# Optimization experiments

Measured on AMD Instinct MI355X. Metric: run time of the kernel, lower is better.

Reference implementation:

```python
import jax, jax.numpy as jnp
import numpy as np

N0, N1 = 20000, 20000     # users, items
F0 = 512                  # raw feature dim per type
HID = 64                  # hidden_dim == H * D
H, D = 8, 8               # num_heads, out_dim
P = 2                     # metapaths per side
E = 200000                # metapath instances per metapath
L = 3                     # metapath length (nodes)
B = 8192                  # link-prediction target batch
AV = 128                  # attn_vec_dim
CH = 128                  # ProductMLP hidden = max(128, HID//2)
ETYPES_USER = [[0, 1], [0, 1]]
ETYPES_ITEM = [[1, 0], [1, 0]]


def setup_inputs() -> dict:
    key = jax.random.key(0)
    ks = jax.random.split(key, 32)
    def nrm(k, shape, fan_in):
        return (jax.random.normal(k, shape, dtype=jnp.float32) * (1.414 / np.sqrt(fan_in))).astype(jnp.float32)
    inp = {}
    inp['feats0'] = jax.random.normal(ks[0], (N0, F0), dtype=jnp.float32)
    inp['feats1'] = jax.random.normal(ks[1], (N1, F0), dtype=jnp.float32)
    for t, off in ((0, 2), (1, 6)):
        inp[f'tower{t}_pw'] = nrm(ks[off], (F0, HID), F0)
        inp[f'tower{t}_pb'] = jnp.zeros((HID,), jnp.float32)
        inp[f'tower{t}_w2'] = nrm(ks[off + 1], (HID, HID), HID)
        inp[f'tower{t}_b2'] = jnp.zeros((HID,), jnp.float32)
        inp[f'tower{t}_g'] = jnp.ones((HID,), jnp.float32)
        inp[f'tower{t}_be'] = jnp.zeros((HID,), jnp.float32)
    inp['r_vec'] = jax.random.normal(ks[10], (2, HID // 2, 2), dtype=jnp.float32)
    inp['attn_user'] = nrm(ks[11], (P, H, D), D)
    inp['attn_item'] = nrm(ks[12], (P, H, D), D)
    inp['su_w1'] = nrm(ks[13], (HID, AV), HID)
    inp['su_b1'] = jnp.zeros((AV,), jnp.float32)
    inp['su_w2'] = nrm(ks[14], (AV,), AV)
    inp['si_w1'] = nrm(ks[15], (HID, AV), HID)
    inp['si_b1'] = jnp.zeros((AV,), jnp.float32)
    inp['si_w2'] = nrm(ks[16], (AV,), AV)
    inp['cw1'] = nrm(ks[17], (HID, CH), HID)
    inp['cb1'] = jnp.zeros((CH,), jnp.float32)
    inp['cw2'] = nrm(ks[18], (CH, 2), CH)
    inp['idx0'] = jnp.arange(N0, dtype=jnp.int32)
    inp['idx1'] = jnp.arange(N1, dtype=jnp.int32) + N0
    inp['emi_user'] = jax.random.randint(ks[20], (P, E, L), 0, N0 + N1, dtype=jnp.int32)
    inp['tgt_user'] = jax.random.randint(ks[21], (P, E), 0, B, dtype=jnp.int32)
    inp['emi_item'] = jax.random.randint(ks[22], (P, E, L), 0, N0 + N1, dtype=jnp.int32)
    inp['tgt_item'] = jax.random.randint(ks[23], (P, E), 0, B, dtype=jnp.int32)
    return inp


def _tower(x, pw, pb, w2, b2, g, be):
    # Linear -> GELU -> Linear -> residual -> LayerNorm (dropout off in eval)
    z = x @ pw + pb
    h = jax.nn.gelu(z, approximate=False)
    h = h @ w2 + b2
    y = h + z
    mu = y.mean(-1, keepdims=True)
    var = ((y - mu) ** 2).mean(-1, keepdims=True)
    return (y - mu) / jnp.sqrt(var + 1e-5) * g + be


def _rot_full(r_vec):
    # normalize to unit complex, then even etypes = r, odd etypes = conj(r)
    r = r_vec / jnp.linalg.norm(r_vec, axis=-1, keepdims=True)
    conj = r * jnp.array([1.0, -1.0], dtype=r.dtype)
    return jnp.stack([r, conj], axis=1).reshape(-1, r.shape[1], 2)  # [num_edge_type, HID//2, 2]


def _final_r(rfull, etypes):
    # cumulative complex rotation applied to each position along the metapath
    fr = [None] * L
    fr[L - 1] = jnp.stack([jnp.ones(HID // 2), jnp.zeros(HID // 2)], axis=1).astype(rfull.dtype)
    for i in range(L - 2, -1, -1):
        rv = rfull[etypes[i]]
        re = fr[i + 1][:, 0] * rv[:, 0] - fr[i + 1][:, 1] * rv[:, 1]
        im = fr[i + 1][:, 0] * rv[:, 1] + fr[i + 1][:, 1] * rv[:, 0]
        fr[i] = jnp.stack([re, im], axis=1)
    return jnp.stack(fr)  # [L, HID//2, 2]


def _metapath(feat, emi, tgt, attn, etypes, rfull):
    # gather node features along each metapath instance: [E, L, HID//2, 2]
    ed = feat[emi].reshape(emi.shape[0], L, HID // 2, 2)
    fr = _final_r(rfull, etypes)  # last position is identity rotation
    re = ed[..., 0] * fr[:, :, 0] - ed[..., 1] * fr[:, :, 1]
    im = ed[..., 0] * fr[:, :, 1] + ed[..., 1] * fr[:, :, 0]
    hidden = jnp.stack([re, im], -1).mean(axis=1).reshape(-1, HID)  # mean over metapath positions
    eft = hidden.reshape(-1, H, D)
    e = jax.nn.leaky_relu((eft * attn).sum(-1), 0.01)  # [E, H]
    # edge softmax over instances sharing a target node
    m = jax.ops.segment_max(e, tgt, num_segments=B)
    m = jnp.where(jnp.isfinite(m), m, 0.0)
    a = jnp.exp(e - m[tgt])
    s = jax.ops.segment_sum(a, tgt, num_segments=B)
    w = a / (s[tgt] + 1e-9)
    ret = jax.ops.segment_sum(w[..., None] * eft, tgt, num_segments=B)  # [B, H, D]
    return jax.nn.elu(ret.reshape(B, HID))


def _semantic(outs, w1, b1, w2):
    hs = jnp.stack(outs)  # [P, B, HID]
    s = (jnp.tanh(hs @ w1 + b1) @ w2).mean(axis=1)  # [P]
    beta = jax.nn.softmax(s)
    return (beta[:, None, None] * hs).sum(0)  # [B, HID]


def reference(feats0, feats1, tower0_pw, tower0_pb, tower0_w2, tower0_b2, tower0_g, tower0_be,
              tower1_pw, tower1_pb, tower1_w2, tower1_b2, tower1_g, tower1_be,
              r_vec, attn_user, attn_item, su_w1, su_b1, su_w2, si_w1, si_b1, si_w2,
              cw1, cb1, cw2, idx0, idx1, emi_user, tgt_user, emi_item, tgt_item):
    t0 = _tower(feats0, tower0_pw, tower0_pb, tower0_w2, tower0_b2, tower0_g, tower0_be)
    t1 = _tower(feats1, tower1_pw, tower1_pb, tower1_w2, tower1_b2, tower1_g, tower1_be)
    feat = jnp.zeros((N0 + N1, HID), jnp.float32).at[idx0].set(t0).at[idx1].set(t1)
    rfull = _rot_full(r_vec)
    user_outs = [_metapath(feat, emi_user[p], tgt_user[p], attn_user[p], ETYPES_USER[p], rfull) for p in range(P)]
    item_outs = [_metapath(feat, emi_item[p], tgt_item[p], attn_item[p], ETYPES_ITEM[p], rfull) for p in range(P)]
    h_user = _semantic(user_outs, su_w1, su_b1, su_w2)
    h_item = _semantic(item_outs, si_w1, si_b1, si_w2)
    x = h_user * h_item
    h = jax.nn.relu(x @ cw1 + cb1)
    logits = h @ cw2
    return jax.nn.softmax(logits, axis=-1)
```

## Files before the change

### kernel.cpp

```cpp
#include <hip/hip_runtime.h>
#include <hip/hip_bf16.h>
#include <math.h>

#define NN0 20000
#define NN1 20000
#define NTOT 40000
#define FF0 512
#define HIDD 64
#define EEE 200000
#define BBB 8192
#define AVV 128
#define CHH 128

typedef __bf16 bf16x8 __attribute__((ext_vector_type(8)));
typedef __bf16 bf16x4 __attribute__((ext_vector_type(4)));
typedef float f32x4 __attribute__((ext_vector_type(4)));
typedef float f32x2 __attribute__((ext_vector_type(2)));

__device__ __forceinline__ float fast_tanh(float x) {
    float e2 = __expf(2.f * x);
    return 1.f - 2.f / (e2 + 1.f);
}

__device__ __forceinline__ f32x2 bf2_to_f32x2(unsigned int c) {
    f32x2 r;
    r.x = __uint_as_float(c << 16);
    r.y = __uint_as_float(c & 0xffff0000u);
    return r;
}

__device__ __forceinline__ void coarse_prefix(const int* __restrict__ cnt32p, int combo, int tid,
                                              int& cv, int& excl) {
    cv = cnt32p[(combo * 32 + tid) * 32];
    int pre = cv;
#pragma unroll
    for (int d = 1; d < 32; d <<= 1) {
        int o = __shfl_up(pre, d);
        if (tid >= d) pre += o;
    }
    excl = pre - cv;
}

#define HCHUNK 1024
__global__ __launch_bounds__(256) void prep_hist(
    const float* __restrict__ pw0, const float* __restrict__ pw1,
    const float* __restrict__ w20, const float* __restrict__ w21,
    __bf16* __restrict__ wprep, __bf16* __restrict__ w2prep,
    const int* __restrict__ tgt_user, const int* __restrict__ tgt_item,
    int* __restrict__ cnt32p)
{
    __shared__ int ch[32];
    int bx = blockIdx.x;
    if (bx < 16) {
        int tw = bx & 1, seg = bx >> 1;
        const float* w = tw ? pw1 : pw0;
        __bf16* base = wprep + tw * 65536;
        for (int idx = seg * 4096 + threadIdx.x; idx < (seg + 1) * 4096; idx += 256) {
            int k = idx >> 6, n = idx & 63;
            float v = w[idx];
            __bf16 hi = (__bf16)v;
            __bf16 lo = (__bf16)(v - (float)hi);
            int ks = k >> 5, kb = (k >> 3) & 3, j = k & 7;
            int nt = n >> 4, fr = n & 15;
            int lane = kb * 16 + fr;
            int off = ((ks * 4 + nt) * 64 + lane) * 8 + j;
            base[off] = hi;
            base[32768 + off] = lo;
        }
        const float* w2 = tw ? w21 : w20;
        __bf16* base2 = w2prep + tw * 8192;
        for (int idx = seg * 512 + threadIdx.x; idx < (seg + 1) * 512; idx += 256) {
            int k = idx >> 6, n = idx & 63;
            float v = w2[idx];
            __bf16 hi = (__bf16)v;
            __bf16 lo = (__bf16)(v - (float)hi);
            int ks = k >> 5, kb = (k >> 3) & 3, j = k & 7;
            int nt = n >> 4, fr = n & 15;
            int lane = kb * 16 + fr;
            int off = ((ks * 4 + nt) * 64 + lane) * 8 + j;
            base2[off] = hi;
            base2[4096 + off] = lo;
        }
    } else {
        int flat = bx - 16;
        int combo = flat & 3, blk = flat >> 2;
        const int* tgt = (combo < 2 ? tgt_user : tgt_item) + (long)(combo & 1) * EEE;
        int tid = threadIdx.x;
        if (tid < 32) ch[tid] = 0;
        __syncthreads();
        int base = blk * HCHUNK;
#pragma unroll
        for (int q = 0; q < 4; q++) {
            int i = base + q * 256 + tid;
            if (i < EEE) atomicAdd(&ch[tgt[i] >> 8], 1);
        }
        __syncthreads();
        if (tid < 32 && ch[tid]) atomicAdd(&cnt32p[(combo * 32 + tid) * 32], ch[tid]);
    }
}

#define CHUNKF 1024
__global__ __launch_bounds__(128) void tower_binA(
    const float* __restrict__ x0, const float* __restrict__ x1,
    const __bf16* __restrict__ wprep, const __bf16* __restrict__ w2prep,
    const float* __restrict__ pb0, const float* __restrict__ pb1,
    const float* __restrict__ b20, const float* __restrict__ b21,
    const float* __restrict__ g0, const float* __restrict__ g1,
    const float* __restrict__ be0, const float* __restrict__ be1,
    const int* __restrict__ idxa, const int* __restrict__ idxb,
    __hip_bfloat16* __restrict__ feat,
    const int* __restrict__ tgt_user, const int* __restrict__ tgt_item,
    const int* __restrict__ emi_user, const int* __restrict__ emi_item,
    const int* __restrict__ cnt32p, int* __restrict__ cur32cnt,
    ushort4* __restrict__ binbuf)
{
    __shared__ __align__(16) char pool[8960];
    int bx = blockIdx.x;
    if (bx < 2500) {
        int tile = bx >> 1, tw = bx & 1;
        const float* x  = tw ? x1 : x0;
        const float* pb = tw ? pb1 : pb0;
        const float* b2 = tw ? b21 : b20;
        const float* g  = tw ? g1 : g0;
        const float* be = tw ? be1 : be0;
        const int* idx  = tw ? idxb : idxa;
        float (*hs)[68] = (float(*)[68])pool;
        float* pq  = (float*)(pool + 4352);
        float* pq2 = (float*)(pool + 4480);

        int wv = threadIdx.x >> 6;
        int l = threadIdx.x & 63;
        int fr = l & 15, kb = l >> 4;
        int nt0 = 2 * wv;
        int row0 = tile * 16;
        const float* xp = x + (long)(row0 + fr) * FF0 + kb * 8;
        const __bf16* bp = wprep + tw * 65536;

        f32x4 acc[2];
#pragma unroll
        for (int n2 = 0; n2 < 2; n2++) acc[n2] = (f32x4){0.f, 0.f, 0.f, 0.f};

        float4 a0c, a1c, a0n, a1n;
        bf16x8 bhc[2], blc[2], bhn[2], bln[2];

        a0c = *(const float4*)xp;
        a1c = *(const float4*)(xp + 4);
#pragma unroll
        for (int n2 = 0; n2 < 2; n2++) {
            bhc[n2] = *(const bf16x8*)(bp + ((nt0 + n2) * 64 + l) * 8);
            blc[n2] = *(const bf16x8*)(bp + 32768 + ((nt0 + n2) * 64 + l) * 8);
        }

#pragma unroll 2
        for (int ks = 0; ks < 16; ks++) {
            if (ks + 1 < 16) {
                a0n = *(const float4*)(xp + (ks + 1) * 32);
                a1n = *(const float4*)(xp + (ks + 1) * 32 + 4);
#pragma unroll
                for (int n2 = 0; n2 < 2; n2++) {
                    bhn[n2] = *(const bf16x8*)(bp + (((ks + 1) * 4 + nt0 + n2) * 64 + l) * 8);
                    bln[n2] = *(const bf16x8*)(bp + 32768 + (((ks + 1) * 4 + nt0 + n2) * 64 + l) * 8);
                }
            }
            __builtin_amdgcn_sched_barrier(0);
            float av[8] = {a0c.x, a0c.y, a0c.z, a0c.w, a1c.x, a1c.y, a1c.z, a1c.w};
            bf16x8 ah, al;
#pragma unroll
            for (int j = 0; j < 8; j++) {
                __bf16 h = (__bf16)av[j];
                ah[j] = h;
                al[j] = (__bf16)(av[j] - (float)h);
            }
#pragma unroll
            for (int n2 = 0; n2 < 2; n2++) {
                acc[n2] = __builtin_amdgcn_mfma_f32_16x16x32_bf16(ah, bhc[n2], acc[n2], 0, 0, 0);
                acc[n2] = __builtin_amdgcn_mfma_f32_16x16x32_bf16(al, bhc[n2], acc[n2], 0, 0, 0);
                acc[n2] = __builtin_amdgcn_mfma_f32_16x16x32_bf16(ah, blc[n2], acc[n2], 0, 0, 0);
            }
            a0c = a0n; a1c = a1n;
#pragma unroll
            for (int n2 = 0; n2 < 2; n2++) { bhc[n2] = bhn[n2]; blc[n2] = bln[n2]; }
        }

        float pbv[2], b2v[2];
#pragma unroll
        for (int n2 = 0; n2 < 2; n2++) {
            pbv[n2] = pb[(nt0 + n2) * 16 + fr];
            b2v[n2] = b2[(nt0 + n2) * 16 + fr];
        }
        f32x4 acc2[2];
#pragma unroll
        for (int n2 = 0; n2 < 2; n2++) {
#pragma unroll
            for (int j = 0; j < 4; j++) {
                float z = acc[n2][j] + pbv[n2];
                float h = 0.5f * z * (1.f + erff(z * 0.70710678118654752f));
                hs[kb * 4 + j][(nt0 + n2) * 16 + fr] = h;
                acc2[n2][j] = z + b2v[n2];
            }
        }
        __syncthreads();

        const __bf16* w2p = w2prep + tw * 8192;
#pragma unroll
        for (int ks = 0; ks < 2; ks++) {
            float4 h0 = *(const float4*)&hs[fr][ks * 32 + kb * 8];
            float4 h1 = *(const float4*)&hs[fr][ks * 32 + kb * 8 + 4];
            float hv[8] = {h0.x, h0.y, h0.z, h0.w, h1.x, h1.y, h1.z, h1.w};
            bf16x8 ah, al;
#pragma unroll
            for (int j = 0; j < 8; j++) {
                __bf16 h = (__bf16)hv[j];
                ah[j] = h;
                al[j] = (__bf16)(hv[j] - (float)h);
            }
#pragma unroll
            for (int n2 = 0; n2 < 2; n2++) {
                bf16x8 bh2 = *(const bf16x8*)(w2p + ((ks * 4 + nt0 + n2) * 64 + l) * 8);
                bf16x8 bl2 = *(const bf16x8*)(w2p + 4096 + ((ks * 4 + nt0 + n2) * 64 + l) * 8);
                acc2[n2] = __builtin_amdgcn_mfma_f32_16x16x32_bf16(ah, bh2, acc2[n2], 0, 0, 0);
                acc2[n2] = __builtin_amdgcn_mfma_f32_16x16x32_bf16(al, bh2, acc2[n2], 0, 0, 0);
                acc2[n2] = __builtin_amdgcn_mfma_f32_16x16x32_bf16(ah, bl2, acc2[n2], 0, 0, 0);
            }
        }

        float pj[4];
#pragma unroll
        for (int j = 0; j < 4; j++) {
            float p = acc2[0][j] + acc2[1][j];
            p += __shfl_xor(p, 1); p += __shfl_xor(p, 2);
            p += __shfl_xor(p, 4); p += __shfl_xor(p, 8);
            pj[j] = p;
        }
        if (fr == 0) {
#pragma unroll
            for (int j = 0; j < 4; j++) pq[wv * 16 + kb * 4 + j] = pj[j];
        }
        __syncthreads();
        float mu[4];
#pragma unroll
        for (int j = 0; j < 4; j++)
            mu[j] = (pj[j] + pq[(wv ^ 1) * 16 + kb * 4 + j]) * (1.f / 64.f);
        float d[2][4], vj[4];
#pragma unroll
        for (int j = 0; j < 4; j++) {
            d[0][j] = acc2[0][j] - mu[j];
            d[1][j] = acc2[1][j] - mu[j];
            float v = d[0][j] * d[0][j] + d[1][j] * d[1][j];
            v += __shfl_xor(v, 1); v += __shfl_xor(v, 2);
            v += __shfl_xor(v, 4); v += __shfl_xor(v, 8);
            vj[j] = v;
        }
        if (fr == 0) {
#pragma unroll
            for (int j = 0; j < 4; j++) pq2[wv * 16 + kb * 4 + j] = vj[j];
        }
        __syncthreads();
        float gv[2], bev[2];
#pragma unroll
        for (int n2 = 0; n2 < 2; n2++) {
            gv[n2] = g[(nt0 + n2) * 16 + fr];
            bev[n2] = be[(nt0 + n2) * 16 + fr];
        }
#pragma unroll
        for (int j = 0; j < 4; j++) {
            float var = (vj[j] + pq2[(wv ^ 1) * 16 + kb * 4 + j]) * (1.f / 64.f);
            float is = 1.f / sqrtf(var + 1e-5f);
#pragma unroll
            for (int n2 = 0; n2 < 2; n2++)
                hs[kb * 4 + j][(nt0 + n2) * 16 + fr] = d[n2][j] * is * gv[n2] + bev[n2];
        }
        __syncthreads();
#pragma unroll
        for (int r = 0; r < 8; r++) {
            int rr = wv * 8 + r;
            feat[(long)idx[row0 + rr] * HIDD + l] = __float2bfloat16(hs[rr][l]);
        }
    } else {
        int flat = bx - 2500;
        int combo = flat & 3;
        int base = (flat >> 2) * CHUNKF;
        const int* tgt = (combo < 2 ? tgt_user : tgt_item) + (long)(combo & 1) * EEE;
        const int* emi = (combo < 2 ? emi_user : emi_item) + (long)(combo & 1) * EEE * 3;
        ushort4* sbuf = (ushort4*)pool;
        int* lcnt  = (int*)(pool + 8192);
        int* lofs  = lcnt + 32;
        int* gbase = lofs + 33;
        int* lcur  = gbase + 32;
        int tid = threadIdx.x;
        if (tid < 32) { lcnt[tid] = 0; lcur[tid] = 0; }
        __syncthreads();
        ushort4 ent[8]; int bk[8];
#pragma unroll
        for (int ps = 0; ps < 8; ps++) {
            int i = base + ps * 128 + tid;
            if (i < EEE) {
                int t = tgt[i];
                ent[ps] = make_ushort4((unsigned short)emi[3 * i], (unsigned short)emi[3 * i + 1],
                                       (unsigned short)emi[3 * i + 2], (unsigned short)t);
                bk[ps] = t >> 8;
                atomicAdd(&lcnt[bk[ps]], 1);
            } else bk[ps] = -1;
        }
        __syncthreads();
        if (tid == 0) {
            int run = 0;
            for (int k = 0; k < 32; k++) { lofs[k] = run; run += lcnt[k]; }
            lofs[32] = run;
        }
        __syncthreads();
        if (tid < 32) {
            int cv, excl;
            coarse_prefix(cnt32p, combo, tid, cv, excl);
            gbase[tid] = excl + atomicAdd(&cur32cnt[combo * 32 + tid], lcnt[tid]);
        }
        __syncthreads();
#pragma unroll
        for (int ps = 0; ps < 8; ps++) {
            if (bk[ps] >= 0) {
                int pos = lofs[bk[ps]] + atomicAdd(&lcur[bk[ps]], 1);
                sbuf[pos] = ent[ps];
            }
        }
        __syncthreads();
        int total = lofs[32];
        ushort4* dst = binbuf + (long)combo * EEE;
        for (int j = tid; j < total; j += 128) {
            ushort4 e = sbuf[j];
            int k = e.w >> 8;
            dst[gbase[k] + (j - lofs[k])] = e;
        }
    }
}

#define BKCAP 7680
__global__ __launch_bounds__(256) void binB_kernel(
    const int* __restrict__ cnt32p, int* __restrict__ offs,
    const ushort4* __restrict__ binbuf, ushort4* __restrict__ nodes)
{
    int combo = blockIdx.y;
    int k = blockIdx.x;
    __shared__ ushort4 sbuf[BKCAP];
    __shared__ int lh[256];
    __shared__ int part[256];
    __shared__ int cex[32], ccn[32];
    int tid = threadIdx.x;
    if (tid < 32) {
        int cv, excl;
        coarse_prefix(cnt32p, combo, tid, cv, excl);
        cex[tid] = excl;
        ccn[tid] = cv;
    }
    lh[tid] = 0;
    __syncthreads();
    int rbeg = cex[k];
    int cnt = ccn[k];
    if (cnt > BKCAP) cnt = BKCAP;
    const ushort4* src = binbuf + (long)combo * EEE + rbeg;
    for (int j = tid; j < cnt; j += 256)
        atomicAdd(&lh[src[j].w & 255], 1);
    __syncthreads();
    int myc = lh[tid];
    part[tid] = myc;
    __syncthreads();
    for (int d = 1; d < 256; d <<= 1) {
        int u = (tid >= d) ? part[tid - d] : 0;
        __syncthreads();
        part[tid] += u;
        __syncthreads();
    }
    int myofs = part[tid] - myc;
    offs[combo * (BBB + 1) + (k << 8) + tid] = rbeg + myofs;
    if (k == 31 && tid == 0) offs[combo * (BBB + 1) + BBB] = EEE;
    __syncthreads();
    lh[tid] = myofs;
    part[tid] = 0;
    __syncthreads();
    for (int j = tid; j < cnt; j += 256) {
        ushort4 e = src[j];
        int b = e.w & 255;
        int pos = lh[b] + atomicAdd(&part[b], 1);
        if (pos < BKCAP) sbuf[pos] = e;
    }
    __syncthreads();
    ushort4* dst = nodes + (long)combo * EEE + rbeg;
    for (int j = tid; j < cnt; j += 256) dst[j] = sbuf[j];
}

__global__ __launch_bounds__(256) void flash_mp(
    const __hip_bfloat16* __restrict__ feat, const ushort4* __restrict__ nodes,
    const int* __restrict__ offs, const float* __restrict__ r_vec,
    const float* __restrict__ attn_user, const float* __restrict__ attn_item,
    float* __restrict__ ret)
{
    int combo = blockIdx.y;
    int wid = threadIdx.x >> 6, lane = threadIdx.x & 63;
    int half = lane >> 5, p = lane & 31;
    int side = combo >> 1;
    const float* attn = (side == 0 ? attn_user : attn_item) + (combo & 1) * 64;
    const unsigned int* f2 = (const unsigned int*)feat;
    float2 rb = ((const float2*)r_vec)[p];
    float invn = 1.f / sqrtf(rb.x * rb.x + rb.y * rb.y);
    float rvx = rb.x * invn, rvy = rb.y * invn;
    if (side == 0) rvy = -rvy;
    float aRe = attn[2 * p], aIm = attn[2 * p + 1];
    f32x2 av  = { aRe * (1.f / 3.f), aIm * (1.f / 3.f) };
    f32x2 apv = { (rvx * aRe + rvy * aIm) * (1.f / 3.f),
                  (rvx * aIm - rvy * aRe) * (1.f / 3.f) };
    int t = blockIdx.x * 4 + wid;
    const int* of = offs + combo * (BBB + 1);
    int beg = of[t], end = of[t + 1];
    int n = end - beg;
    const ushort4* nd = nodes + (long)combo * EEE;

    float m = -3.4e38f, s = 0.f;
    f32x2 A02 = {0.f, 0.f}, A1 = {0.f, 0.f};

    unsigned int c0[4], c1[4], c2[4];
    ushort4 nq[4];
    if (n > 0) {
#pragma unroll
        for (int q = 0; q < 4; q++) {
            ushort4 a = nd[min(beg + 2 * q + half, EEE - 1)];
            c0[q] = f2[(int)a.x * 32 + p];
            c1[q] = f2[(int)a.y * 32 + p];
            c2[q] = f2[(int)a.z * 32 + p];
        }
#pragma unroll
        for (int q = 0; q < 4; q++)
            nq[q] = nd[min(beg + 8 + 2 * q + half, EEE - 1)];
    }
    for (int it = 0; it < n; it += 8) {
        f32x2 u1[4], v02[4];
        float e[4];
#pragma unroll
        for (int q = 0; q < 4; q++) {
            f32x2 u0 = bf2_to_f32x2(c0[q]);
            u1[q]    = bf2_to_f32x2(c1[q]);
            f32x2 u2 = bf2_to_f32x2(c2[q]);
            v02[q] = u0 + u2;
        }
        if (it + 8 < n) {
#pragma unroll
            for (int q = 0; q < 4; q++) {
                c0[q] = f2[(int)nq[q].x * 32 + p];
                c1[q] = f2[(int)nq[q].y * 32 + p];
                c2[q] = f2[(int)nq[q].z * 32 + p];
            }
#pragma unroll
            for (int q = 0; q < 4; q++)
                nq[q] = nd[min(beg + it + 16 + 2 * q + half, EEE - 1)];
        }
#pragma unroll
        for (int q = 0; q < 4; q++) {
            f32x2 tt = v02[q] * av + u1[q] * apv;
            float pa = tt.x + tt.y;
            pa += __shfl_xor(pa, 1);
            pa += __shfl_xor(pa, 2);
            e[q] = fmaxf(pa, 0.01f * pa);
        }
        if (it + 8 > n) {
#pragma unroll
            for (int q = 0; q < 4; q++)
                if (it + 2 * q + half >= n) e[q] = -3.4e38f;
        }
        float mx = fmaxf(fmaxf(e[0], e[1]), fmaxf(e[2], e[3]));
        float mn = fmaxf(m, fmaxf(mx, __shfl_xor(mx, 32)));
        float alpha = __expf(m - mn);
        s *= alpha; A02 *= alpha; A1 *= alpha;
        float wl = 0.f;
#pragma unroll
        for (int q = 0; q < 4; q++) {
            float w = __expf(e[q] - mn);
            wl += w;
            A02 += v02[q] * w;
            A1  += u1[q] * w;
        }
        s += wl + __shfl_xor(wl, 32);
        m = mn;
    }
    float Sx = A02.x + __shfl_xor(A02.x, 32);
    float Sy = A02.y + __shfl_xor(A02.y, 32);
    float Tx = A1.x + __shfl_xor(A1.x, 32);
    float Ty = A1.y + __shfl_xor(A1.y, 32);
    float inv = (1.f / 3.f) / (s + 1e-9f);
    float vx = (Sx + rvx * Tx - rvy * Ty) * inv;
    float vy = (Sy + rvx * Ty + rvy * Tx) * inv;
    vx = vx > 0.f ? vx : __expf(vx) - 1.f;
    vy = vy > 0.f ? vy : __expf(vy) - 1.f;
    if (half == 0)
        ((float2*)ret)[((long)combo * BBB + t) * 32 + p] = make_float2(vx, vy);
}

__global__ __launch_bounds__(256) void sem_kernel(
    const float* __restrict__ ret,
    const float* __restrict__ su_w1, const float* __restrict__ su_b1, const float* __restrict__ su_w2,
    const float* __restrict__ si_w1, const float* __restrict__ si_b1, const float* __restrict__ si_w2,
    float* __restrict__ s_acc)
{
    int combo = blockIdx.y;
    int side = combo >> 1;
    const float* w1 = side ? si_w1 : su_w1;
    const float* b1 = side ? si_b1 : su_b1;
    const float* w2 = side ? si_w2 : su_w2;
    __shared__ float vs[64][68];
    __shared__ float w1s[64][128];
    int tid = threadIdx.x;
    int rowbase = blockIdx.x * 64;
    const float4* r4 = (const float4*)ret;
    for (int li = tid; li < 1024; li += 256) {
        int r = li >> 4, c4 = li & 15;
        float4 v = r4[((long)combo * BBB + rowbase + r) * 16 + c4];
        *(float4*)&vs[r][c4 * 4] = v;
    }
    const float4* w14 = (const float4*)w1;
    for (int li = tid; li < 2048; li += 256) {
        float4 v = w14[li];
        *(float4*)&w1s[li >> 5][(li & 31) * 4] = v;
    }
    __syncthreads();
    int ct = tid & 15, rt = tid >> 4;
    float acc[4][8];
#pragma unroll
    for (int cc = 0; cc < 8; cc++) {
        float b = b1[8 * ct + cc];
#pragma unroll
        for (int j = 0; j < 4; j++) acc[j][cc] = b;
    }
    for (int k = 0; k < 64; k += 4) {
        float4 xv[4];
#pragma unroll
        for (int j = 0; j < 4; j++) xv[j] = *(const float4*)&vs[4 * rt + j][k];
#pragma unroll
        for (int kk = 0; kk < 4; kk++) {
            float4 wv0 = *(const float4*)&w1s[k + kk][8 * ct];
            float4 wv1 = *(const float4*)&w1s[k + kk][8 * ct + 4];
#pragma unroll
            for (int j = 0; j < 4; j++) {
                float xx = kk == 0 ? xv[j].x : kk == 1 ? xv[j].y : kk == 2 ? xv[j].z : xv[j].w;
                acc[j][0] = fmaf(xx, wv0.x, acc[j][0]);
                acc[j][1] = fmaf(xx, wv0.y, acc[j][1]);
                acc[j][2] = fmaf(xx, wv0.z, acc[j][2]);
                acc[j][3] = fmaf(xx, wv0.w, acc[j][3]);
                acc[j][4] = fmaf(xx, wv1.x, acc[j][4]);
                acc[j][5] = fmaf(xx, wv1.y, acc[j][5]);
                acc[j][6] = fmaf(xx, wv1.z, acc[j][6]);
                acc[j][7] = fmaf(xx, wv1.w, acc[j][7]);
            }
        }
    }
    float tot = 0.f;
#pragma unroll
    for (int cc = 0; cc < 8; cc++) {
        float w2v = w2[8 * ct + cc];
#pragma unroll
        for (int j = 0; j < 4; j++) tot += fast_tanh(acc[j][cc]) * w2v;
    }
    for (int off = 32; off; off >>= 1) tot += __shfl_xor(tot, off);
    __shared__ float red[4];
    int lane = tid & 63, wid = tid >> 6;
    if (lane == 0) red[wid] = tot;
    __syncthreads();
    if (tid == 0) atomicAdd(&s_acc[combo], red[0] + red[1] + red[2] + red[3]);
}

__global__ __launch_bounds__(256) void final_kernel(
    const float* __restrict__ ret, const float* __restrict__ s_acc,
    const float* __restrict__ cw1, const float* __restrict__ cb1, const float* __restrict__ cw2,
    float* __restrict__ outp)
{
    float s0 = s_acc[0] * (1.f / BBB), s1 = s_acc[1] * (1.f / BBB);
    float s2 = s_acc[2] * (1.f / BBB), s3 = s_acc[3] * (1.f / BBB);
    float mu = fmaxf(s0, s1);
    float e0 = __expf(s0 - mu), e1 = __expf(s1 - mu);
    float bu0 = e0 / (e0 + e1), bu1 = e1 / (e0 + e1);
    float mi = fmaxf(s2, s3);
    float f0 = __expf(s2 - mi), f1 = __expf(s3 - mi);
    float bi0 = f0 / (f0 + f1), bi1 = f1 / (f0 + f1);

    __shared__ float xsld[64][68];
    __shared__ float w1s[64][128];
    int tid = threadIdx.x;
    int rowbase = blockIdx.x * 64;
    const float4* r4 = (const float4*)ret;
    for (int li = tid; li < 1024; li += 256) {
        int r = li >> 4, c4 = li & 15;
        float4 a = r4[((long)0 * BBB + rowbase + r) * 16 + c4];
        float4 b = r4[((long)1 * BBB + rowbase + r) * 16 + c4];
        float4 cc = r4[((long)2 * BBB + rowbase + r) * 16 + c4];
        float4 d = r4[((long)3 * BBB + rowbase + r) * 16 + c4];
        float4 xv;
        xv.x = (bu0 * a.x + bu1 * b.x) * (bi0 * cc.x + bi1 * d.x);
        xv.y = (bu0 * a.y + bu1 * b.y) * (bi0 * cc.y + bi1 * d.y);
        xv.z = (bu0 * a.z + bu1 * b.z) * (bi0 * cc.z + bi1 * d.z);
        xv.w = (bu0 * a.w + bu1 * b.w) * (bi0 * cc.w + bi1 * d.w);
        *(float4*)&xsld[r][c4 * 4] = xv;
    }
    const float4* w14 = (const float4*)cw1;
    for (int li = tid; li < 2048; li += 256) {
        float4 v = w14[li];
        *(float4*)&w1s[li >> 5][(li & 31) * 4] = v;
    }
    __syncthreads();
    int ct = tid & 15, rt = tid >> 4;
    float acc[4][8];
#pragma unroll
    for (int cc = 0; cc < 8; cc++) {
        float b = cb1[8 * ct + cc];
#pragma unroll
        for (int j = 0; j < 4; j++) acc[j][cc] = b;
    }
    for (int k = 0; k < 64; k += 4) {
        float4 xv[4];
#pragma unroll
        for (int j = 0; j < 4; j++) xv[j] = *(const float4*)&xsld[4 * rt + j][k];
#pragma unroll
        for (int kk = 0; kk < 4; kk++) {
            float4 wv0 = *(const float4*)&w1s[k + kk][8 * ct];
            float4 wv1 = *(const float4*)&w1s[k + kk][8 * ct + 4];
#pragma unroll
            for (int j = 0; j < 4; j++) {
                float xx = kk == 0 ? xv[j].x : kk == 1 ? xv[j].y : kk == 2 ? xv[j].z : xv[j].w;
                acc[j][0] = fmaf(xx, wv0.x, acc[j][0]);
                acc[j][1] = fmaf(xx, wv0.y, acc[j][1]);
                acc[j][2] = fmaf(xx, wv0.z, acc[j][2]);
                acc[j][3] = fmaf(xx, wv0.w, acc[j][3]);
                acc[j][4] = fmaf(xx, wv1.x, acc[j][4]);
                acc[j][5] = fmaf(xx, wv1.y, acc[j][5]);
                acc[j][6] = fmaf(xx, wv1.z, acc[j][6]);
                acc[j][7] = fmaf(xx, wv1.w, acc[j][7]);
            }
        }
    }
    float pp0[4], pp1[4];
#pragma unroll
    for (int j = 0; j < 4; j++) { pp0[j] = 0.f; pp1[j] = 0.f; }
#pragma unroll
    for (int cc = 0; cc < 8; cc++) {
        int col = 8 * ct + cc;
        float c0 = cw2[col * 2], c1 = cw2[col * 2 + 1];
#pragma unroll
        for (int j = 0; j < 4; j++) {
            float h = fmaxf(acc[j][cc], 0.f);
            pp0[j] = fmaf(h, c0, pp0[j]);
            pp1[j] = fmaf(h, c1, pp1[j]);
        }
    }
    __syncthreads();
    float2* red = (float2*)xsld;
#pragma unroll
    for (int j = 0; j < 4; j++)
        red[(4 * rt + j) * 16 + ct] = make_float2(pp0[j], pp1[j]);
    __syncthreads();
    if (tid < 64) {
        float q0 = 0.f, q1 = 0.f;
        for (int i = 0; i < 16; i++) {
            float2 e = red[tid * 16 + i];
            q0 += e.x; q1 += e.y;
        }
        float mx = fmaxf(q0, q1);
        float a0 = __expf(q0 - mx), a1 = __expf(q1 - mx);
        float dn = a0 + a1;
        outp[(rowbase + tid) * 2] = a0 / dn;
        outp[(rowbase + tid) * 2 + 1] = a1 / dn;
    }
}

extern "C" void kernel_launch(void* const* d_in, const int* in_sizes, int n_in,
                              void* d_out, int out_size, void* d_ws, size_t ws_size,
                              hipStream_t stream)
{
    const float* feats0 = (const float*)d_in[0];
    const float* feats1 = (const float*)d_in[1];
    const float* t0_pw = (const float*)d_in[2];
    const float* t0_pb = (const float*)d_in[3];
    const float* t0_w2 = (const float*)d_in[4];
    const float* t0_b2 = (const float*)d_in[5];
    const float* t0_g  = (const float*)d_in[6];
    const float* t0_be = (const float*)d_in[7];
    const float* t1_pw = (const float*)d_in[8];
    const float* t1_pb = (const float*)d_in[9];
    const float* t1_w2 = (const float*)d_in[10];
    const float* t1_b2 = (const float*)d_in[11];
    const float* t1_g  = (const float*)d_in[12];
    const float* t1_be = (const float*)d_in[13];
    const float* r_vec = (const float*)d_in[14];
    const float* attn_user = (const float*)d_in[15];
    const float* attn_item = (const float*)d_in[16];
    const float* su_w1 = (const float*)d_in[17];
    const float* su_b1 = (const float*)d_in[18];
    const float* su_w2 = (const float*)d_in[19];
    const float* si_w1 = (const float*)d_in[20];
    const float* si_b1 = (const float*)d_in[21];
    const float* si_w2 = (const float*)d_in[22];
    const float* cw1 = (const float*)d_in[23];
    const float* cb1 = (const float*)d_in[24];
    const float* cw2 = (const float*)d_in[25];
    const int* idx0 = (const int*)d_in[26];
    const int* idx1 = (const int*)d_in[27];
    const int* emi_user = (const int*)d_in[28];
    const int* tgt_user = (const int*)d_in[29];
    const int* emi_item = (const int*)d_in[30];
    const int* tgt_item = (const int*)d_in[31];
    float* outp = (float*)d_out;

    char* ws = (char*)d_ws;
    __hip_bfloat16* feat = (__hip_bfloat16*)(ws + 0);
    int*     cnt32p  = (int*)(ws + 5120000);
    int*     cur32cnt= (int*)(ws + 5136384);
    float*   s_acc   = (float*)(ws + 5136896);
    int*     offs    = (int*)(ws + 5137408);
    ushort4* binbuf  = (ushort4*)(ws + 5268736);
    ushort4* nodes   = (ushort4*)(ws + 11668736);
    float*   ret_buf = (float*)(ws + 18068736);
    __bf16*  wprep   = (__bf16*)(ws + 26457344);
    __bf16*  w2prep  = (__bf16*)(ws + 11668736);

    hipMemsetAsync(cnt32p, 0, 16384 + 512 + 256, stream);

    prep_hist<<<16 + 4 * ((EEE + HCHUNK - 1) / HCHUNK), 256, 0, stream>>>(
        t0_pw, t1_pw, t0_w2, t1_w2, wprep, w2prep, tgt_user, tgt_item, cnt32p);

    tower_binA<<<2500 + 4 * ((EEE + CHUNKF - 1) / CHUNKF), 128, 0, stream>>>(
        feats0, feats1, wprep, w2prep, t0_pb, t1_pb,
        t0_b2, t1_b2, t0_g, t1_g, t0_be, t1_be, idx0, idx1, feat,
        tgt_user, tgt_item, emi_user, emi_item, cnt32p, cur32cnt, binbuf);

    binB_kernel<<<dim3(32, 4), 256, 0, stream>>>(cnt32p, offs, binbuf, nodes);

    flash_mp<<<dim3(BBB / 4, 4), 256, 0, stream>>>(feat, nodes, offs, r_vec,
                                                   attn_user, attn_item, ret_buf);

    sem_kernel<<<dim3(BBB / 64, 4), 256, 0, stream>>>(ret_buf, su_w1, su_b1, su_w2,
                                                      si_w1, si_b1, si_w2, s_acc);
    final_kernel<<<BBB / 64, 256, 0, stream>>>(ret_buf, s_acc, cw1, cb1, cw2, outp);
}
```

Baseline: 292.5 us.

## Vectorize weight prep, drop sched barrier, widen binB blocks to 512 threads

```diff
diff --git a/kernel.cpp b/kernel.cpp
--- a/kernel.cpp
+++ b/kernel.cpp
@@ -51,38 +51,46 @@
 {
     __shared__ int ch[32];
     int bx = blockIdx.x;
-    if (bx < 16) {
-        int tw = bx & 1, seg = bx >> 1;
+    if (bx < 32) {
+        int tw = bx & 1;
+        int c2 = (bx >> 1) * 256 + threadIdx.x;
         const float* w = tw ? pw1 : pw0;
+        int ksnt = c2 >> 6, lane = c2 & 63;
+        int ks = ksnt >> 2, nt = ksnt & 3;
+        int kb = lane >> 4, fr = lane & 15;
+        const float* src = w + (ks * 32 + kb * 8) * 64 + nt * 16 + fr;
+        bf16x8 hi, lo;
+#pragma unroll
+        for (int j = 0; j < 8; j++) {
+            float v = src[j * 64];
+            __bf16 h = (__bf16)v;
+            hi[j] = h;
+            lo[j] = (__bf16)(v - (float)h);
+        }
         __bf16* base = wprep + tw * 65536;
-        for (int idx = seg * 4096 + threadIdx.x; idx < (seg + 1) * 4096; idx += 256) {
-            int k = idx >> 6, n = idx & 63;
-            float v = w[idx];
-            __bf16 hi = (__bf16)v;
-            __bf16 lo = (__bf16)(v - (float)hi);
-            int ks = k >> 5, kb = (k >> 3) & 3, j = k & 7;
-            int nt = n >> 4, fr = n & 15;
-            int lane = kb * 16 + fr;
-            int off = ((ks * 4 + nt) * 64 + lane) * 8 + j;
-            base[off] = hi;
-            base[32768 + off] = lo;
-        }
+        *(bf16x8*)(base + c2 * 8) = hi;
+        *(bf16x8*)(base + 32768 + c2 * 8) = lo;
+    } else if (bx < 36) {
+        int tw = bx & 1;
+        int c2 = ((bx - 32) >> 1) * 256 + threadIdx.x;
         const float* w2 = tw ? w21 : w20;
+        int ksnt = c2 >> 6, lane = c2 & 63;
+        int ks = ksnt >> 2, nt = ksnt & 3;
+        int kb = lane >> 4, fr = lane & 15;
+        const float* src = w2 + (ks * 32 + kb * 8) * 64 + nt * 16 + fr;
+        bf16x8 hi, lo;
+#pragma unroll
+        for (int j = 0; j < 8; j++) {
+            float v = src[j * 64];
+            __bf16 h = (__bf16)v;
+            hi[j] = h;
+            lo[j] = (__bf16)(v - (float)h);
+        }
         __bf16* base2 = w2prep + tw * 8192;
-        for (int idx = seg * 512 + threadIdx.x; idx < (seg + 1) * 512; idx += 256) {
-            int k = idx >> 6, n = idx & 63;
-            float v = w2[idx];
-            __bf16 hi = (__bf16)v;
-            __bf16 lo = (__bf16)(v - (float)hi);
-            int ks = k >> 5, kb = (k >> 3) & 3, j = k & 7;
-            int nt = n >> 4, fr = n & 15;
-            int lane = kb * 16 + fr;
-            int off = ((ks * 4 + nt) * 64 + lane) * 8 + j;
-            base2[off] = hi;
-            base2[4096 + off] = lo;
-        }
+        *(bf16x8*)(base2 + c2 * 8) = hi;
+        *(bf16x8*)(base2 + 4096 + c2 * 8) = lo;
     } else {
-        int flat = bx - 16;
+        int flat = bx - 36;
         int combo = flat & 3, blk = flat >> 2;
         const int* tgt = (combo < 2 ? tgt_user : tgt_item) + (long)(combo & 1) * EEE;
         int tid = threadIdx.x;
@@ -162,7 +170,6 @@
                     bln[n2] = *(const bf16x8*)(bp + 32768 + (((ks + 1) * 4 + nt0 + n2) * 64 + l) * 8);
                 }
             }
-            __builtin_amdgcn_sched_barrier(0);
             float av[8] = {a0c.x, a0c.y, a0c.z, a0c.w, a1c.x, a1c.y, a1c.z, a1c.w};
             bf16x8 ah, al;
 #pragma unroll
@@ -334,7 +341,7 @@
 }
 
 #define BKCAP 7680
-__global__ __launch_bounds__(256) void binB_kernel(
+__global__ __launch_bounds__(512) void binB_kernel(
     const int* __restrict__ cnt32p, int* __restrict__ offs,
     const ushort4* __restrict__ binbuf, ushort4* __restrict__ nodes)
 {
@@ -351,32 +358,34 @@
         cex[tid] = excl;
         ccn[tid] = cv;
     }
-    lh[tid] = 0;
+    if (tid < 256) lh[tid] = 0;
     __syncthreads();
     int rbeg = cex[k];
     int cnt = ccn[k];
     if (cnt > BKCAP) cnt = BKCAP;
     const ushort4* src = binbuf + (long)combo * EEE + rbeg;
-    for (int j = tid; j < cnt; j += 256)
+    for (int j = tid; j < cnt; j += 512)
         atomicAdd(&lh[src[j].w & 255], 1);
     __syncthreads();
-    int myc = lh[tid];
-    part[tid] = myc;
+    int myc = 0;
+    if (tid < 256) { myc = lh[tid]; part[tid] = myc; }
     __syncthreads();
     for (int d = 1; d < 256; d <<= 1) {
-        int u = (tid >= d) ? part[tid - d] : 0;
-        __syncthreads();
-        part[tid] += u;
-        __syncthreads();
-    }
-    int myofs = part[tid] - myc;
-    offs[combo * (BBB + 1) + (k << 8) + tid] = rbeg + myofs;
+        int u = (tid < 256 && tid >= d) ? part[tid - d] : 0;
+        __syncthreads();
+        if (tid < 256) part[tid] += u;
+        __syncthreads();
+    }
+    int myofs = 0;
+    if (tid < 256) {
+        myofs = part[tid] - myc;
+        offs[combo * (BBB + 1) + (k << 8) + tid] = rbeg + myofs;
+    }
     if (k == 31 && tid == 0) offs[combo * (BBB + 1) + BBB] = EEE;
     __syncthreads();
-    lh[tid] = myofs;
-    part[tid] = 0;
-    __syncthreads();
-    for (int j = tid; j < cnt; j += 256) {
+    if (tid < 256) { lh[tid] = myofs; part[tid] = 0; }
+    __syncthreads();
+    for (int j = tid; j < cnt; j += 512) {
         ushort4 e = src[j];
         int b = e.w & 255;
         int pos = lh[b] + atomicAdd(&part[b], 1);
@@ -384,7 +393,7 @@
     }
     __syncthreads();
     ushort4* dst = nodes + (long)combo * EEE + rbeg;
-    for (int j = tid; j < cnt; j += 256) dst[j] = sbuf[j];
+    for (int j = tid; j < cnt; j += 512) dst[j] = sbuf[j];
 }
 
 __global__ __launch_bounds__(256) void flash_mp(
@@ -718,7 +727,7 @@
 
     hipMemsetAsync(cnt32p, 0, 16384 + 512 + 256, stream);
 
-    prep_hist<<<16 + 4 * ((EEE + HCHUNK - 1) / HCHUNK), 256, 0, stream>>>(
+    prep_hist<<<36 + 4 * ((EEE + HCHUNK - 1) / HCHUNK), 256, 0, stream>>>(
         t0_pw, t1_pw, t0_w2, t1_w2, wprep, w2prep, tgt_user, tgt_item, cnt32p);
 
     tower_binA<<<2500 + 4 * ((EEE + CHUNKF - 1) / CHUNKF), 128, 0, stream>>>(
@@ -726,7 +735,7 @@
         t0_b2, t1_b2, t0_g, t1_g, t0_be, t1_be, idx0, idx1, feat,
         tgt_user, tgt_item, emi_user, emi_item, cnt32p, cur32cnt, binbuf);
 
-    binB_kernel<<<dim3(32, 4), 256, 0, stream>>>(cnt32p, offs, binbuf, nodes);
+    binB_kernel<<<dim3(32, 4), 512, 0, stream>>>(cnt32p, offs, binbuf, nodes);
 
     flash_mp<<<dim3(BBB / 4, 4), 256, 0, stream>>>(feat, nodes, offs, r_vec,
                                                    attn_user, attn_item, ret_buf);
```

After: 281.3 us. 1.04x faster.
